# Performance work log

Hardware: AMD Instinct MI355X
Metric: run time of the kernel (lower is better)

The kernel has to match this reference:

```python
import jax, jax.numpy as jnp
import numpy as np

B, T, C, H = 4, 2048, 1024, 16
D = C // H  # head dim = 64

def precompute_rope(dim, max_pos):
    # rope_cache[t, i] = (cos(t*theta_i), sin(t*theta_i)), theta_i = 10000^(-2i/dim)
    i = jnp.arange(dim // 2, dtype=jnp.float32)
    theta = 1.0 / (10000.0 ** (2.0 * i / dim))
    t = jnp.arange(max_pos, dtype=jnp.float32)[:, None]
    ang = t * theta[None, :]
    return jnp.stack([jnp.cos(ang), jnp.sin(ang)], axis=-1)  # (max_pos, dim/2, 2)

def apply_rope(x, rope):
    # x: (B, H, T, D); complex multiply rope * x over pairs of channels
    Tq = x.shape[2]
    xr = x.reshape(x.shape[0], x.shape[1], Tq, D // 2, 2)
    a, b = xr[..., 0], xr[..., 1]
    c = rope[:Tq, :, 0]  # (T, D/2)
    s = rope[:Tq, :, 1]
    real = a * c - b * s
    imag = a * s + b * c
    return jnp.stack([real, imag], axis=-1).reshape(x.shape)

def setup_inputs() -> dict:
    key = jax.random.key(0)
    ks = jax.random.split(key, 9)
    scale = 1.0 / np.sqrt(C)
    def w(k):
        return jax.random.uniform(k, (C, C), jnp.float32, -scale, scale)
    def bvec(k):
        return jax.random.uniform(k, (C,), jnp.float32, -scale, scale)
    return {
        "x": jax.random.normal(ks[0], (B, T, C), jnp.float32),
        "Wq": w(ks[1]), "bq": bvec(ks[2]),
        "Wk": w(ks[3]), "bk": bvec(ks[4]),
        "Wv": w(ks[5]), "bv": bvec(ks[6]),
        "Wp": w(ks[7]), "bp": bvec(ks[8]),
        "rope_cache": precompute_rope(D, T),
    }

def reference(x, Wq, bq, Wk, bk, Wv, bv, Wp, bp, rope_cache):
    B_, T_, C_ = x.shape
    def heads(y):
        return y.reshape(B_, T_, H, D).transpose(0, 2, 1, 3)  # (B,H,T,D)
    q = heads(x @ Wq.T + bq)
    k = heads(x @ Wk.T + bk)
    v = heads(x @ Wv.T + bv)
    q = apply_rope(q, rope_cache)
    k = apply_rope(k, rope_cache)
    att = jnp.einsum("bhqd,bhkd->bhqk", q, k) * (1.0 / np.sqrt(D))
    causal = jnp.tril(jnp.ones((T_, T_), dtype=bool))
    att = jnp.where(causal, att, jnp.float32(-1e10))
    att = jax.nn.softmax(att, axis=-1)
    y = jnp.einsum("bhqk,bhkd->bhqd", att, v)
    y = y.transpose(0, 2, 1, 3).reshape(B_, T_, C_)
    return y @ Wp.T + bp
```

## Files before the change

### kernel.cpp

```cpp
#include <hip/hip_runtime.h>

#define DEVINL __device__ __forceinline__

typedef unsigned short u16;
typedef __attribute__((ext_vector_type(4))) short s16x4;
typedef __attribute__((ext_vector_type(8))) short s16x8;
typedef __attribute__((ext_vector_type(4))) float f32x4;

static constexpr int Bb = 4, Tt = 2048, Cc = 1024, Hh = 16, Dd = 64;
static constexpr int Mm = Bb * Tt;
static constexpr int KK = Cc;

DEVINL float bf2f(u16 u) { return __uint_as_float(((unsigned)u) << 16); }
DEVINL u16 f2bf(float f) {
  unsigned b = __float_as_uint(f);
  b += 0x7fff + ((b >> 16) & 1);
  return (u16)(b >> 16);
}
DEVINL unsigned cvtpk(float lo, float hi) {
  unsigned r;
  asm("v_cvt_pk_bf16_f32 %0, %1, %2" : "=v"(r) : "v"(lo), "v"(hi));
  return r;
}

#define GLDS(gsrc, ldst) \
  __builtin_amdgcn_global_load_lds((const __attribute__((address_space(1))) void*)(gsrc), \
                                   (__attribute__((address_space(3))) void*)(ldst), 16, 0, 0)

__global__ void cvt_bf16(const float* __restrict__ src, u16* __restrict__ dst, int n4) {
  int i = blockIdx.x * blockDim.x + threadIdx.x;
  int st = gridDim.x * blockDim.x;
  for (int g = i; g < n4; g += st) {
    float4 v = ((const float4*)src)[g];
    uint2 o;
    o.x = (unsigned)f2bf(v.x) | ((unsigned)f2bf(v.y) << 16);
    o.y = (unsigned)f2bf(v.z) | ((unsigned)f2bf(v.w) << 16);
    ((uint2*)dst)[g] = o;
  }
}

struct Cvt4Args { const float* s[4]; u16* d[4]; };
__global__ void cvt4(Cvt4Args a, int n4) {
  const float* __restrict__ src = a.s[blockIdx.y];
  u16* __restrict__ dst = a.d[blockIdx.y];
  int i = blockIdx.x * blockDim.x + threadIdx.x;
  int st = gridDim.x * blockDim.x;
  for (int g = i; g < n4; g += st) {
    float4 v = ((const float4*)src)[g];
    uint2 o;
    o.x = (unsigned)f2bf(v.x) | ((unsigned)f2bf(v.y) << 16);
    o.y = (unsigned)f2bf(v.z) | ((unsigned)f2bf(v.w) << 16);
    ((uint2*)dst)[g] = o;
  }
}

__global__ void rope_kernel(u16* __restrict__ q, u16* __restrict__ k,
                            const float* __restrict__ cache) {
  const float CS = 0.18033688f;
  const int total = Bb * Hh * Tt * 8;
  int i = blockIdx.x * blockDim.x + threadIdx.x;
  int st = gridDim.x * blockDim.x;
  for (int g = i; g < total; g += st) {
    int off = g * 8;
    int t = (off >> 6) & (Tt - 1);
    int d0 = off & 63;
    const float* cp = cache + t * 64 + d0;
    float4 c0 = *(const float4*)cp;
    float4 c1 = *(const float4*)(cp + 4);
    float cs[8] = {c0.x, c0.y, c0.z, c0.w, c1.x, c1.y, c1.z, c1.w};
    s16x8 qv = *(s16x8*)(q + off);
    s16x8 kv = *(s16x8*)(k + off);
    s16x8 qo, ko;
#pragma unroll
    for (int p = 0; p < 4; ++p) {
      float c = cs[2 * p], s = cs[2 * p + 1];
      float a = bf2f((u16)qv[2 * p]), b = bf2f((u16)qv[2 * p + 1]);
      qo[2 * p] = (short)f2bf((a * c - b * s) * CS);
      qo[2 * p + 1] = (short)f2bf((a * s + b * c) * CS);
      a = bf2f((u16)kv[2 * p]); b = bf2f((u16)kv[2 * p + 1]);
      ko[2 * p] = (short)f2bf(a * c - b * s);
      ko[2 * p + 1] = (short)f2bf(a * s + b * c);
    }
    *(s16x8*)(q + off) = qo;
    *(s16x8*)(k + off) = ko;
  }
}

#define GEMM_PROLOG()                                              \
  const int tid = threadIdx.x, w = tid >> 6, l = tid & 63;         \
  const int lr = l & 15, lg = l >> 4;                              \
  const int m0 = blockIdx.x * 128, n0 = blockIdx.y * 128;          \
  const int wr = w >> 1, wc = w & 1;                               \
  f32x4 zero = {0.f, 0.f, 0.f, 0.f};                               \
  f32x4 acc[4][4];                                                 \
  _Pragma("unroll") for (int i = 0; i < 4; ++i)                    \
      _Pragma("unroll") for (int j = 0; j < 4; ++j) acc[i][j] = zero; \
  const int srow = l >> 3;                                         \
  const int scolsw = ((l & 7) ^ (l >> 3)) * 8;

#define GEMM_KLOOP(Aptr, Wptr)                                                         \
  for (int k0 = 0; k0 < KK; k0 += 64) {                                                \
    _Pragma("unroll") for (int i = 0; i < 4; ++i) {                                    \
      int row = i * 32 + w * 8 + srow;                                                 \
      GLDS(Aptr + (size_t)(m0 + row) * KK + k0 + scolsw, &As[(i * 32 + w * 8) * 64]);  \
      GLDS(Wptr + (size_t)(n0 + row) * KK + k0 + scolsw, &Bs[(i * 32 + w * 8) * 64]);  \
    }                                                                                  \
    __syncthreads();                                                                   \
    _Pragma("unroll") for (int kk = 0; kk < 2; ++kk) {                                 \
      s16x8 af[4], bfr[4];                                                             \
      _Pragma("unroll") for (int i = 0; i < 4; ++i)                                    \
          af[i] = *(const s16x8*)&As[(wr * 64 + i * 16 + lr) * 64 +                    \
                                     ((kk * 32 + lg * 8) ^ ((lr & 7) << 3))];          \
      _Pragma("unroll") for (int j = 0; j < 4; ++j)                                    \
          bfr[j] = *(const s16x8*)&Bs[(wc * 64 + j * 16 + lr) * 64 +                   \
                                      ((kk * 32 + lg * 8) ^ ((lr & 7) << 3))];         \
      _Pragma("unroll") for (int i = 0; i < 4; ++i)                                    \
          _Pragma("unroll") for (int j = 0; j < 4; ++j)                                \
              acc[i][j] =                                                              \
                  __builtin_amdgcn_mfma_f32_16x16x32_bf16(af[i], bfr[j], acc[i][j], 0, 0, 0); \
    }                                                                                  \
    __syncthreads();                                                                   \
  }

__global__ __launch_bounds__(256) void gemm_qk(const u16* __restrict__ A,
                                               const u16* __restrict__ W0,
                                               const u16* __restrict__ W1,
                                               const float* __restrict__ b0,
                                               const float* __restrict__ b1,
                                               u16* __restrict__ O0, u16* __restrict__ O1) {
  __shared__ __align__(16) u16 As[128 * 64];
  __shared__ __align__(16) u16 Bs[128 * 64];
  const int z = blockIdx.z;
  const u16* __restrict__ Wt = z ? W1 : W0;
  const float* __restrict__ bias = z ? b1 : b0;
  u16* __restrict__ O = z ? O1 : O0;
  GEMM_PROLOG()
  GEMM_KLOOP(A, Wt)
#pragma unroll
  for (int j = 0; j < 4; ++j) {
    int ncol = n0 + wc * 64 + j * 16 + lr;
    float bj = bias[ncol];
    int hh = ncol >> 6, dd = ncol & 63;
#pragma unroll
    for (int i = 0; i < 4; ++i) {
#pragma unroll
      for (int r = 0; r < 4; ++r) {
        int mrow = m0 + wr * 64 + i * 16 + lg * 4 + r;
        int bb2 = mrow >> 11, tt2 = mrow & (Tt - 1);
        O[(((size_t)bb2 * Hh + hh) * Tt + tt2) * Dd + dd] = f2bf(acc[i][j][r] + bj);
      }
    }
  }
}

__global__ __launch_bounds__(256) void gemm_v(const u16* __restrict__ A,
                                              const u16* __restrict__ Wt,
                                              const float* __restrict__ bias,
                                              u16* __restrict__ O) {
  __shared__ __align__(16) u16 As[128 * 64];
  __shared__ __align__(16) u16 Bs[128 * 64];
  __shared__ __align__(16) u16 Ts[128 * 64];
  GEMM_PROLOG()
  GEMM_KLOOP(A, Wt)
  const int bb2 = m0 >> 11, tloc = m0 & (Tt - 1);
#pragma unroll
  for (int p = 0; p < 2; ++p) {
    if (p) __syncthreads();
    if (wr == p) {
#pragma unroll
      for (int j = 0; j < 4; ++j) {
        int ncl = wc * 64 + j * 16 + lr;
        float bj = bias[n0 + ncl];
        int xw = (ncl & 3) << 2;
#pragma unroll
        for (int i = 0; i < 4; ++i) {
          s16x4 pk;
#pragma unroll
          for (int r = 0; r < 4; ++r) pk[r] = (short)f2bf(acc[i][j][r] + bj);
          *(s16x4*)&Ts[ncl * 64 + (((i * 4 + lg) ^ xw) << 2)] = pk;
        }
      }
    }
    __syncthreads();
    const int rn = tid >> 3, t8 = tid & 7;
#pragma unroll
    for (int it = 0; it < 4; ++it) {
      int rown = it * 32 + rn;
      int slot = (t8 * 2) ^ ((rown & 3) << 2);
      s16x8 v = *(const s16x8*)&Ts[rown * 64 + slot * 4];
      int ncol = n0 + rown;
      int hh2 = ncol >> 6, dd = ncol & 63;
      *(s16x8*)&O[(((size_t)bb2 * Hh + hh2) * Dd + dd) * Tt + tloc + p * 64 + t8 * 8] = v;
    }
  }
}

__global__ __launch_bounds__(256) void gemm_proj(const u16* __restrict__ A,
                                                 const u16* __restrict__ Wt,
                                                 const float* __restrict__ bias,
                                                 float* __restrict__ O) {
  __shared__ __align__(16) u16 As[128 * 64];
  __shared__ __align__(16) u16 Bs[128 * 64];
  GEMM_PROLOG()
  GEMM_KLOOP(A, Wt)
#pragma unroll
  for (int j = 0; j < 4; ++j) {
    int ncol = n0 + wc * 64 + j * 16 + lr;
    float bj = bias[ncol];
#pragma unroll
    for (int i = 0; i < 4; ++i) {
#pragma unroll
      for (int r = 0; r < 4; ++r) {
        int mrow = m0 + wr * 64 + i * 16 + lg * 4 + r;
        O[(size_t)mrow * Cc + ncol] = acc[i][j][r] + bj;
      }
    }
  }
}

__global__ __launch_bounds__(256, 4) void attn_kernel(const u16* __restrict__ Q,
                                                      const u16* __restrict__ K,
                                                      const u16* __restrict__ VTg,
                                                      u16* __restrict__ Out) {
  __shared__ __align__(16) u16 Ks[128 * 64];
  __shared__ __align__(16) u16 VTs[64 * 128];
  __shared__ __align__(16) u16 Ps[4 * 16 * 32];
  const int tid = threadIdx.x, w = tid >> 6, l = tid & 63;
  const int lr = l & 15, lg = l >> 4;
  const int bh = blockIdx.y;
  const size_t base = (size_t)bh * Tt * Dd;
  const u16* Qp = Q + base;
  const u16* Kp = K + base;
  const u16* Vp = VTg + base;
  const int bb2 = bh >> 4, hh = bh & 15;
  const float NEG = -3.0e9f;
  f32x4 zero = {0.f, 0.f, 0.f, 0.f};
  const int krow_l = l >> 3, kc8sw = ((l & 7) ^ (l >> 3)) * 8;
  const int vrow_l = l >> 4, vc8 = l & 15;
  const int psw = (lr >> 1) & 3;

  auto process = [&](int qt) {
    const int qb0 = qt * 64;
    const int qrow = qb0 + w * 16 + lr;
    const int qg = qrow;
    s16x8 qf[2];
    qf[0] = *(const s16x8*)(Qp + (size_t)qrow * 64 + lg * 8);
    qf[1] = *(const s16x8*)(Qp + (size_t)qrow * 64 + 32 + lg * 8);
    f32x4 o[4] = {zero, zero, zero, zero};
    float m = -3e38f, lsum = 0.f;
    const int ktiles = (qt + 2) >> 1;
    for (int kt = 0; kt < ktiles; ++kt) {
      const int kk0 = kt * 128;
#pragma unroll
      for (int i = 0; i < 4; ++i) {
        int krow = i * 32 + w * 8 + krow_l;
        GLDS(Kp + (size_t)(kk0 + krow) * 64 + kc8sw, &Ks[(i * 32 + w * 8) * 64]);
        int d = i * 16 + w * 4 + vrow_l;
        GLDS(Vp + (size_t)d * Tt + kk0 + ((vc8 ^ (d & 7)) * 8), &VTs[(i * 16 + w * 4) * 128]);
      }
      __syncthreads();
      float pv[8][4];
      const int diag = (kt == ktiles - 1);
      __builtin_amdgcn_s_setprio(1);
#pragma unroll
      for (int cf = 0; cf < 8; ++cf) {
        f32x4 s = zero;
#pragma unroll
        for (int kf = 0; kf < 2; ++kf) {
          s16x8 kb = *(const s16x8*)&Ks[(cf * 16 + lr) * 64 + (((kf * 4 + lg) ^ (lr & 7)) << 3)];
          s = __builtin_amdgcn_mfma_f32_16x16x32_bf16(kb, qf[kf], s, 0, 0, 0);
        }
        if (diag) {
          int key0 = kk0 + cf * 16 + lg * 4;
#pragma unroll
          for (int r = 0; r < 4; ++r) pv[cf][r] = (key0 + r <= qg) ? s[r] : NEG;
        } else {
#pragma unroll
          for (int r = 0; r < 4; ++r) pv[cf][r] = s[r];
        }
      }
      __builtin_amdgcn_s_setprio(0);
      float t0 = fmaxf(fmaxf(pv[0][0], pv[0][1]), fmaxf(pv[0][2], pv[0][3]));
#pragma unroll
      for (int cf = 1; cf < 8; ++cf) {
        float tc = fmaxf(fmaxf(pv[cf][0], pv[cf][1]), fmaxf(pv[cf][2], pv[cf][3]));
        t0 = fmaxf(t0, tc);
      }
      t0 = fmaxf(t0, __shfl_xor(t0, 16));
      float tm = fmaxf(t0, __shfl_xor(t0, 32));
      int stable = tm <= m + 11.5f;
      if (!__all(stable)) {
        float mn = fmaxf(m, tm);
        float fsc = __builtin_amdgcn_exp2f(m - mn);
        lsum *= fsc;
        m = mn;
#pragma unroll
        for (int jf = 0; jf < 4; ++jf) {
          o[jf][0] *= fsc; o[jf][1] *= fsc; o[jf][2] *= fsc; o[jf][3] *= fsc;
        }
      }
      float psum = 0.f;
#pragma unroll
      for (int cf = 0; cf < 8; ++cf)
#pragma unroll
        for (int r = 0; r < 4; ++r) {
          float p = __builtin_amdgcn_exp2f(pv[cf][r] - m);
          pv[cf][r] = p;
          psum += p;
        }
      psum += __shfl_xor(psum, 16);
      psum += __shfl_xor(psum, 32);
      lsum += psum;
#pragma unroll
      for (int kk = 0; kk < 4; ++kk) {
#pragma unroll
        for (int c = 0; c < 2; ++c) {
          int cf = kk * 2 + c;
          unsigned w0 = cvtpk(pv[cf][0], pv[cf][1]);
          unsigned w1 = cvtpk(pv[cf][2], pv[cf][3]);
          int col0 = c * 16 + lg * 4;
          int idx = w * 512 + lr * 32 + ((((col0 >> 3) ^ psw)) << 3) + (col0 & 7);
          *(unsigned*)&Ps[idx] = w0;
          *(unsigned*)&Ps[idx + 2] = w1;
        }
        s16x8 pa = *(const s16x8*)&Ps[w * 512 + lr * 32 + ((lg ^ psw) << 3)];
        __builtin_amdgcn_s_setprio(1);
#pragma unroll
        for (int jf = 0; jf < 4; ++jf) {
          s16x8 vb = *(const s16x8*)&VTs[(jf * 16 + lr) * 128 + (((kk * 4 + lg) ^ (lr & 7)) << 3)];
          o[jf] = __builtin_amdgcn_mfma_f32_16x16x32_bf16(vb, pa, o[jf], 0, 0, 0);
        }
        __builtin_amdgcn_s_setprio(0);
      }
      __syncthreads();
    }
    float linv = 1.0f / lsum;
    int tq = qb0 + w * 16 + lr;
    u16* orow = Out + ((size_t)(bb2 * Tt + tq)) * Cc + hh * 64 + lg * 4;
#pragma unroll
    for (int jf = 0; jf < 4; ++jf) {
      uint2 pk;
      pk.x = cvtpk(o[jf][0] * linv, o[jf][1] * linv);
      pk.y = cvtpk(o[jf][2] * linv, o[jf][3] * linv);
      *(uint2*)&orow[jf * 16] = pk;
    }
  };

  process(blockIdx.x);
  process(31 - blockIdx.x);
}

extern "C" void kernel_launch(void* const* d_in, const int* in_sizes, int n_in,
                              void* d_out, int out_size, void* d_ws, size_t ws_size,
                              hipStream_t stream) {
  (void)in_sizes; (void)n_in; (void)out_size; (void)ws_size;
  const float* x = (const float*)d_in[0];
  const float* Wq = (const float*)d_in[1];
  const float* bq = (const float*)d_in[2];
  const float* Wk = (const float*)d_in[3];
  const float* bk = (const float*)d_in[4];
  const float* Wv = (const float*)d_in[5];
  const float* bv = (const float*)d_in[6];
  const float* Wp = (const float*)d_in[7];
  const float* bp = (const float*)d_in[8];
  const float* rope = (const float*)d_in[9];

  char* ws = (char*)d_ws;
  const size_t MB = 1024 * 1024;
  u16* xb  = (u16*)(ws + 0);
  u16* wqb = (u16*)(ws + 16 * MB);
  u16* wkb = (u16*)(ws + 18 * MB);
  u16* wvb = (u16*)(ws + 20 * MB);
  u16* wpb = (u16*)(ws + 22 * MB);
  u16* qb  = (u16*)(ws + 24 * MB);
  u16* kb  = (u16*)(ws + 40 * MB);
  u16* vt  = (u16*)(ws + 56 * MB);
  u16* att = (u16*)(ws + 72 * MB);

  cvt_bf16<<<2048, 256, 0, stream>>>(x, xb, (Mm * Cc) / 4);
  Cvt4Args ca;
  ca.s[0] = Wq; ca.s[1] = Wk; ca.s[2] = Wv; ca.s[3] = Wp;
  ca.d[0] = wqb; ca.d[1] = wkb; ca.d[2] = wvb; ca.d[3] = wpb;
  cvt4<<<dim3(256, 4), 256, 0, stream>>>(ca, (Cc * Cc) / 4);

  gemm_qk<<<dim3(Mm / 128, Cc / 128, 2), 256, 0, stream>>>(xb, wqb, wkb, bq, bk, qb, kb);
  gemm_v<<<dim3(Mm / 128, Cc / 128), 256, 0, stream>>>(xb, wvb, bv, vt);

  rope_kernel<<<2048, 256, 0, stream>>>(qb, kb, rope);

  attn_kernel<<<dim3(16, Bb * Hh), 256, 0, stream>>>(qb, kb, vt, att);

  gemm_proj<<<dim3(Mm / 128, Cc / 128), 256, 0, stream>>>(att, wpb, bp, (float*)d_out);
}
```

Measured before the change: 214.4 us.

## Double-buffer 64-key K/V tiles in attention and remap block-to-head order

```diff
diff --git a/kernel.cpp b/kernel.cpp
--- a/kernel.cpp
+++ b/kernel.cpp
@@ -222,12 +222,14 @@
                                                       const u16* __restrict__ K,
                                                       const u16* __restrict__ VTg,
                                                       u16* __restrict__ Out) {
-  __shared__ __align__(16) u16 Ks[128 * 64];
-  __shared__ __align__(16) u16 VTs[64 * 128];
+  __shared__ __align__(16) u16 Ks[2][64 * 64];
+  __shared__ __align__(16) u16 VTs[2][64 * 64];
   __shared__ __align__(16) u16 Ps[4 * 16 * 32];
   const int tid = threadIdx.x, w = tid >> 6, l = tid & 63;
   const int lr = l & 15, lg = l >> 4;
-  const int bh = blockIdx.y;
+  const int n = blockIdx.x + 16 * blockIdx.y;
+  const int bh = ((n & 7) << 3) + (n >> 7);
+  const int qpair = (n >> 3) & 15;
   const size_t base = (size_t)bh * Tt * Dd;
   const u16* Qp = Q + base;
   const u16* Kp = K + base;
@@ -236,7 +238,6 @@
   const float NEG = -3.0e9f;
   f32x4 zero = {0.f, 0.f, 0.f, 0.f};
   const int krow_l = l >> 3, kc8sw = ((l & 7) ^ (l >> 3)) * 8;
-  const int vrow_l = l >> 4, vc8 = l & 15;
   const int psw = (lr >> 1) & 3;
 
   auto process = [&](int qt) {
@@ -248,30 +249,41 @@
     qf[1] = *(const s16x8*)(Qp + (size_t)qrow * 64 + 32 + lg * 8);
     f32x4 o[4] = {zero, zero, zero, zero};
     float m = -3e38f, lsum = 0.f;
-    const int ktiles = (qt + 2) >> 1;
+    const int ktiles = qt + 1;
+    auto stage = [&](int kt, int buf) {
+      const int kk0 = kt * 64;
+#pragma unroll
+      for (int i = 0; i < 2; ++i) {
+        int row = i * 32 + w * 8 + krow_l;
+        GLDS(Kp + (size_t)(kk0 + row) * 64 + kc8sw, &Ks[buf][(i * 32 + w * 8) * 64]);
+        GLDS(Vp + (size_t)row * Tt + kk0 + kc8sw, &VTs[buf][(i * 32 + w * 8) * 64]);
+      }
+    };
+    stage(0, 0);
     for (int kt = 0; kt < ktiles; ++kt) {
-      const int kk0 = kt * 128;
-#pragma unroll
-      for (int i = 0; i < 4; ++i) {
-        int krow = i * 32 + w * 8 + krow_l;
-        GLDS(Kp + (size_t)(kk0 + krow) * 64 + kc8sw, &Ks[(i * 32 + w * 8) * 64]);
-        int d = i * 16 + w * 4 + vrow_l;
-        GLDS(Vp + (size_t)d * Tt + kk0 + ((vc8 ^ (d & 7)) * 8), &VTs[(i * 16 + w * 4) * 128]);
-      }
-      __syncthreads();
-      float pv[8][4];
+      const int buf = kt & 1;
+      if (kt + 1 < ktiles) {
+        stage(kt + 1, buf ^ 1);
+        asm volatile("s_waitcnt vmcnt(4)" ::: "memory");
+      } else {
+        asm volatile("s_waitcnt vmcnt(0)" ::: "memory");
+      }
+      __builtin_amdgcn_s_barrier();
+      __builtin_amdgcn_sched_barrier(0);
+      float pv[4][4];
       const int diag = (kt == ktiles - 1);
       __builtin_amdgcn_s_setprio(1);
 #pragma unroll
-      for (int cf = 0; cf < 8; ++cf) {
+      for (int cf = 0; cf < 4; ++cf) {
         f32x4 s = zero;
 #pragma unroll
         for (int kf = 0; kf < 2; ++kf) {
-          s16x8 kb = *(const s16x8*)&Ks[(cf * 16 + lr) * 64 + (((kf * 4 + lg) ^ (lr & 7)) << 3)];
+          s16x8 kb = *(const s16x8*)&Ks[buf][(cf * 16 + lr) * 64 +
+                                            (((kf * 4 + lg) ^ (lr & 7)) << 3)];
           s = __builtin_amdgcn_mfma_f32_16x16x32_bf16(kb, qf[kf], s, 0, 0, 0);
         }
         if (diag) {
-          int key0 = kk0 + cf * 16 + lg * 4;
+          int key0 = kt * 64 + cf * 16 + lg * 4;
 #pragma unroll
           for (int r = 0; r < 4; ++r) pv[cf][r] = (key0 + r <= qg) ? s[r] : NEG;
         } else {
@@ -282,7 +294,7 @@
       __builtin_amdgcn_s_setprio(0);
       float t0 = fmaxf(fmaxf(pv[0][0], pv[0][1]), fmaxf(pv[0][2], pv[0][3]));
 #pragma unroll
-      for (int cf = 1; cf < 8; ++cf) {
+      for (int cf = 1; cf < 4; ++cf) {
         float tc = fmaxf(fmaxf(pv[cf][0], pv[cf][1]), fmaxf(pv[cf][2], pv[cf][3]));
         t0 = fmaxf(t0, tc);
       }
@@ -301,7 +313,7 @@
       }
       float psum = 0.f;
 #pragma unroll
-      for (int cf = 0; cf < 8; ++cf)
+      for (int cf = 0; cf < 4; ++cf)
 #pragma unroll
         for (int r = 0; r < 4; ++r) {
           float p = __builtin_amdgcn_exp2f(pv[cf][r] - m);
@@ -312,7 +324,7 @@
       psum += __shfl_xor(psum, 32);
       lsum += psum;
 #pragma unroll
-      for (int kk = 0; kk < 4; ++kk) {
+      for (int kk = 0; kk < 2; ++kk) {
 #pragma unroll
         for (int c = 0; c < 2; ++c) {
           int cf = kk * 2 + c;
@@ -327,12 +339,14 @@
         __builtin_amdgcn_s_setprio(1);
 #pragma unroll
         for (int jf = 0; jf < 4; ++jf) {
-          s16x8 vb = *(const s16x8*)&VTs[(jf * 16 + lr) * 128 + (((kk * 4 + lg) ^ (lr & 7)) << 3)];
+          s16x8 vb = *(const s16x8*)&VTs[buf][(jf * 16 + lr) * 64 +
+                                             (((kk * 4 + lg) ^ (lr & 7)) << 3)];
           o[jf] = __builtin_amdgcn_mfma_f32_16x16x32_bf16(vb, pa, o[jf], 0, 0, 0);
         }
         __builtin_amdgcn_s_setprio(0);
       }
-      __syncthreads();
+      __builtin_amdgcn_sched_barrier(0);
+      __builtin_amdgcn_s_barrier();
     }
     float linv = 1.0f / lsum;
     int tq = qb0 + w * 16 + lr;
@@ -346,8 +360,8 @@
     }
   };
 
-  process(blockIdx.x);
-  process(31 - blockIdx.x);
+  process(qpair);
+  process(31 - qpair);
 }
 
 extern "C" void kernel_launch(void* const* d_in, const int* in_sizes, int n_in,
```

Result: faster. 185.8 us (-13.4%).
